# Kernel optimization log

Measured on AMD Instinct MI355X. Metric: run time of the kernel, lower is better.

The kernel has to match this reference:

```python
import jax, jax.numpy as jnp
import numpy as np

B, N, HID, EPOCH = 16, 512, 32, 201


def setup_inputs() -> dict:
    key = jax.random.key(0)
    k1, k2, k3, k4 = jax.random.split(key, 4)
    f = jax.random.normal(k1, (B, 1, N, N), dtype=jnp.float32)
    # per-sample 3x3 stencil: perturbed 5-point Laplacian, positive center for stable Jacobi
    base = jnp.array([[0., -1., 0.], [-1., 4., -1.], [0., -1., 0.]], dtype=jnp.float32)
    kernelA = base[None, None] + 0.1 * jax.random.normal(k2, (B, 1, 3, 3), dtype=jnp.float32)
    kernelA = kernelA.at[:, :, 1, 1].set(jnp.maximum(kernelA[:, :, 1, 1], 1.0))
    u = jnp.zeros((B, 1, N, N), jnp.float32)
    # stand-in DeepONet H: pointwise 2 -> HID -> 1 MLP on concat(LFA, residual)
    W1 = 0.1 * jax.random.normal(k3, (HID, 2), dtype=jnp.float32)
    b1 = jnp.zeros((HID,), jnp.float32)
    W2 = 0.1 * jax.random.normal(k4, (1, HID), dtype=jnp.float32)
    b2 = jnp.zeros((1,), jnp.float32)
    return {"f": f, "kernelA": kernelA, "u": u, "W1": W1, "b1": b1, "W2": W2, "b2": b2, "epoch": EPOCH}


def _A(x, kernel):
    # per-sample 3x3 stencil: batch dim mapped to channels, grouped conv (groups = B)
    bsz = x.shape[0]
    y = jax.lax.conv_general_dilated(
        jnp.transpose(x, (1, 0, 2, 3)), kernel, (1, 1), ((1, 1), (1, 1)),
        dimension_numbers=("NCHW", "OIHW", "NCHW"), feature_group_count=bsz)
    return jnp.transpose(y, (1, 0, 2, 3))


def _lfa(kernelA, n):
    # ComputeSmootherFactor: Jacobi symbol |prod_j (1 - tau * A_hat(theta))| on the frequency grid
    h = 1.0 / (n + 1)
    p = np.arange(-(n // 2), n // 2)
    P1, P2 = np.meshgrid(p, p)
    t1 = jnp.asarray(2j * np.pi * h * P1, jnp.complex64)
    t2 = jnp.asarray(2j * np.pi * h * P2, jnp.complex64)
    E = jnp.stack([
        jnp.exp(-t1 - t2), jnp.exp(-t2), jnp.exp(t1 - t2),
        jnp.exp(-t1), jnp.ones_like(t1), jnp.exp(t1),
        jnp.exp(-t1 + t2), jnp.exp(t2), jnp.exp(t1 + t2)])  # [9,N,N]
    bsz = kernelA.shape[0]
    S = jnp.einsum("bk,kxy->bxy", kernelA.reshape(bsz, 9).astype(jnp.complex64), E)
    tau = (0.5 / kernelA[:, 0, 1, 1]).astype(jnp.complex64)[:, None, None]
    y = (1.0 - tau * S) ** 5  # 5 identical Jacobi factors
    return jnp.abs(y)[:, None].astype(jnp.float32)  # [B,1,N,N]


def _H(lfa, r, W1, b1, W2, b2):
    # pointwise MLP correction operator (stand-in for DeepONet)
    z = jnp.concatenate([lfa, r], axis=1)  # [B,2,N,N]
    hdn = jax.nn.gelu(jnp.einsum("bcxy,oc->boxy", z, W1) + b1[None, :, None, None])
    return jnp.einsum("bcxy,oc->boxy", hdn, W2) + b2[None, :, None, None]


def reference(f, kernelA, u, W1, b1, W2, b2, epoch):
    K = (epoch - 1) // 100 + 1
    n = f.shape[-1]
    lfa = _lfa(kernelA, n)
    taus = 0.5 / kernelA[:, :, 1:2, 1:2]  # [B,1,1,1], w=0.5
    x = jnp.zeros_like(f)
    for _ in range(K):
        for _ in range(10):  # jacobi, M=10
            x = x + taus * (f - _A(x, kernelA))
        r = f - _A(x, kernelA)
        x = x + _H(lfa, r, W1, b1, W2, b2)
    r = f - _A(x, kernelA)
    return jnp.linalg.norm(r) / jnp.linalg.norm(f)
```

## Files before the change

kernel.cpp:

```cpp
#include <hip/hip_runtime.h>
#include <math.h>

#define BB 16
#define NN 512
#define HID 32

#define HALO 16
#define TW 96
#define TWP 97
#define OT 64

#define GELU_K1 (-2.302208201f)
#define GELU_K2 (-0.102944244f)

#define TPH 0.012247925f
#define CDR 0.99992499f
#define SDR 0.012247618f

__global__ __launch_bounds__(256) void lfa_kernel(const float* __restrict__ kernelA,
                                                  float* __restrict__ lfa) {
    const int t = threadIdx.x;
    const int strip = t & 127;
    const int i = blockIdx.y * 2 + (t >> 7);
    const int b = blockIdx.z;
    const int j0 = strip * 4;
    const float* a = kernelA + b * 9;
    float a0 = a[0], a1 = a[1], a2 = a[2], a3 = a[3], a4 = a[4];
    float a5 = a[5], a6 = a[6], a7 = a[7], a8 = a[8];
    const float A35 = a3 + a5, A17 = a1 + a7, A08 = a0 + a8, A26 = a2 + a6;
    const float B53 = a5 - a3, B71 = a7 - a1, B80 = a8 - a0, B26 = a2 - a6;
    const float tau = 0.5f / a4;

    float th2 = TPH * (float)(i - NN / 2);
    float th1 = TPH * (float)(j0 - NN / 2);
    float s1, c1, s2, c2;
    sincosf(th1, &s1, &c1);
    sincosf(th2, &s2, &c2);

    float out[4];
#pragma unroll
    for (int k = 0; k < 4; ++k) {
        float cc = c1 * c2, ss = s1 * s2, sc = s1 * c2, cs = c1 * s2;
        float cpp = cc - ss, cpm = cc + ss, spp = sc + cs, spm = sc - cs;
        float re = fmaf(A35, c1, a4); re = fmaf(A17, c2, re);
        re = fmaf(A08, cpp, re);      re = fmaf(A26, cpm, re);
        float im = B53 * s1;          im = fmaf(B71, s2, im);
        im = fmaf(B80, spp, im);      im = fmaf(B26, spm, im);
        float zre = fmaf(-tau, re, 1.0f);
        float zim = tau * im;
        float m2 = fmaf(zre, zre, zim * zim);
        out[k] = m2 * m2 * sqrtf(m2);
        float tt = s1 * SDR;
        float ns = fmaf(s1, CDR, c1 * SDR);
        c1 = fmaf(c1, CDR, -tt);
        s1 = ns;
    }
    float4 ov = {out[0], out[1], out[2], out[3]};
    *(float4*)(lfa + (size_t)b * NN * NN + (size_t)i * NN + j0) = ov;
}

template <bool FIRST>
__global__ __launch_bounds__(256) void fused_cycle(
        const float* __restrict__ xin, float* __restrict__ xout,
        const float* __restrict__ f, const float* __restrict__ kernelA,
        const float* __restrict__ lfa,
        const float* __restrict__ W1, const float* __restrict__ b1,
        const float* __restrict__ W2, const float* __restrict__ b2) {
    __shared__ float sxraw[98 * TWP + 2];
    float* sx = sxraw + TWP + 1;
    const int tx = threadIdx.x;
    const int ty = threadIdx.y;
    const int t  = ty * 32 + tx;
    const int b  = blockIdx.z;
    const int gy0 = blockIdx.y * OT;
    const int gx0 = blockIdx.x * OT;
    const int goi = gy0 - HALO;
    const int goj = gx0 - HALO;
    const float* fg = f + (size_t)b * NN * NN;
    const float* ag = kernelA + b * 9;
    const float ar0 = ag[0], ar1 = ag[1], ar2 = ag[2], ar3 = ag[3], ar4 = ag[4];
    const float ar5 = ag[5], ar6 = ag[6], ar7 = ag[7], ar8 = ag[8];
    const float tau = 0.5f / ar4;
    const float s0 = tau * ar0, q1 = tau * ar1, q2 = tau * ar2, q3 = tau * ar3;
    const float q4 = tau * ar4, q5 = tau * ar5, q6 = tau * ar6, q7 = tau * ar7;
    const float q8 = tau * ar8;

    if (t < 98) sxraw[t] = 0.f;
    if (t < 96) sxraw[97 + 97 * t] = 0.f;
    if (t < 98) sxraw[9409 + t] = 0.f;

    if (!FIRST) {
        const float* xg = xin + (size_t)b * NN * NN;
#pragma unroll
        for (int k = 0; k < (TW * TW) / 256; ++k) {
            int idx = t + k * 256;
            int row = idx / TW, col = idx - row * TW;
            int gi = goi + row, gj = goj + col;
            float v = 0.f;
            if (gi >= 0 && gi < NN && gj >= 0 && gj < NN) v = xg[gi * NN + gj];
            sx[row * TWP + col] = v;
        }
    }

    const int R0 = ty * 12, C0 = tx * 3;

    const float* pb  = sx + (R0 - 1) * TWP + (C0 - 1);
    float*       pwv = sx + R0 * TWP + C0;

    float vR[12], vC[3];
#pragma unroll
    for (int r = 0; r < 12; ++r) {
        int R = R0 + r, gi = goi + R;
        vR[r] = (R >= 1 && R < TW - 1 && gi >= 0 && gi < NN) ? 1.f : 0.f;
    }
#pragma unroll
    for (int c = 0; c < 3; ++c) {
        int C = C0 + c, gj = goj + C;
        vC[c] = (C >= 1 && C < TW - 1 && gj >= 0 && gj < NN) ? 1.f : 0.f;
    }

    float frt[12][3];
#pragma unroll
    for (int r = 0; r < 12; ++r) {
        int gi = goi + R0 + r;
#pragma unroll
        for (int c = 0; c < 3; ++c) {
            int gj = goj + C0 + c;
            frt[r][c] = (gi >= 0 && gi < NN && gj >= 0 && gj < NN)
                            ? tau * fg[gi * NN + gj] : 0.f;
        }
    }

    __syncthreads();

    float cur[12][3];
    if (FIRST) {
#pragma unroll
        for (int r = 0; r < 12; ++r) {
#pragma unroll
            for (int c = 0; c < 3; ++c)
                cur[r][c] = (vR[r] * vC[c]) * frt[r][c];
        }
        pwv[0] = cur[0][0]; pwv[1] = cur[0][1]; pwv[2] = cur[0][2];
        pwv[11 * TWP] = cur[11][0]; pwv[11 * TWP + 1] = cur[11][1];
        pwv[11 * TWP + 2] = cur[11][2];
#pragma unroll
        for (int r = 1; r < 11; ++r) {
            pwv[r * TWP] = cur[r][0];
            pwv[r * TWP + 2] = cur[r][2];
        }
        __syncthreads();
    } else {
#pragma unroll
        for (int r = 0; r < 12; ++r) {
            cur[r][0] = pwv[r * TWP];
            cur[r][1] = pwv[r * TWP + 1];
            cur[r][2] = pwv[r * TWP + 2];
        }
    }

    for (int s = FIRST ? 1 : 0; s < 10; ++s) {
        float top0 = pb[0], top1 = pb[1], top2 = pb[2], top3 = pb[3], top4 = pb[4];
        float bot0 = pb[13 * TWP],     bot1 = pb[13 * TWP + 1],
              bot2 = pb[13 * TWP + 2], bot3 = pb[13 * TWP + 3],
              bot4 = pb[13 * TWP + 4];
        float pm0 = top1, pm1v = top2, pm2 = top3;
        float Lm1 = top0, Rm1 = top4;
        float Lc = pb[TWP], Rc = pb[TWP + 4];
#pragma unroll
        for (int r = 0; r < 12; ++r) {
            float n0, n1, n2, Lp, Rp;
            if (r < 11) {
                n0 = cur[r + 1][0]; n1 = cur[r + 1][1]; n2 = cur[r + 1][2];
                Lp = pb[(r + 2) * TWP];
                Rp = pb[(r + 2) * TWP + 4];
            } else {
                n0 = bot1; n1 = bot2; n2 = bot3; Lp = bot0; Rp = bot4;
            }
            float o0 = cur[r][0], o1 = cur[r][1], o2 = cur[r][2];
            {
                float ax = s0 * Lm1;
                ax = fmaf(q1, pm0, ax); ax = fmaf(q2, pm1v, ax);
                ax = fmaf(q3, Lc, ax);  ax = fmaf(q4, o0, ax);
                ax = fmaf(q5, o1, ax);  ax = fmaf(q6, Lp, ax);
                ax = fmaf(q7, n0, ax);  ax = fmaf(q8, n1, ax);
                cur[r][0] = fmaf(vR[r] * vC[0], frt[r][0] - ax, o0);
            }
            {
                float ax = s0 * pm0;
                ax = fmaf(q1, pm1v, ax); ax = fmaf(q2, pm2, ax);
                ax = fmaf(q3, o0, ax);   ax = fmaf(q4, o1, ax);
                ax = fmaf(q5, o2, ax);   ax = fmaf(q6, n0, ax);
                ax = fmaf(q7, n1, ax);   ax = fmaf(q8, n2, ax);
                cur[r][1] = fmaf(vR[r] * vC[1], frt[r][1] - ax, o1);
            }
            {
                float ax = s0 * pm1v;
                ax = fmaf(q1, pm2, ax); ax = fmaf(q2, Rm1, ax);
                ax = fmaf(q3, o1, ax);  ax = fmaf(q4, o2, ax);
                ax = fmaf(q5, Rc, ax);  ax = fmaf(q6, n1, ax);
                ax = fmaf(q7, n2, ax);  ax = fmaf(q8, Rp, ax);
                cur[r][2] = fmaf(vR[r] * vC[2], frt[r][2] - ax, o2);
            }
            pm0 = o0; pm1v = o1; pm2 = o2;
            Lm1 = Lc; Rm1 = Rc; Lc = Lp; Rc = Rp;
        }
        __syncthreads();
        if (s < 9) {
            pwv[0] = cur[0][0]; pwv[1] = cur[0][1]; pwv[2] = cur[0][2];
            pwv[11 * TWP] = cur[11][0]; pwv[11 * TWP + 1] = cur[11][1];
            pwv[11 * TWP + 2] = cur[11][2];
#pragma unroll
            for (int r = 1; r < 11; ++r) {
                pwv[r * TWP] = cur[r][0];
                pwv[r * TWP + 2] = cur[r][2];
            }
        } else {
#pragma unroll
            for (int r = 0; r < 12; ++r) {
                pwv[r * TWP] = cur[r][0];
                pwv[r * TWP + 1] = cur[r][1];
                pwv[r * TWP + 2] = cur[r][2];
            }
        }
        __syncthreads();
    }

    const int orow = t >> 2;
    const int oseg = t & 3;
    const int Rl = HALO + orow;
    const int Cl0 = HALO + oseg * 16;
    const float* pw = sx + (Rl - 1) * TWP + (Cl0 - 1);
    float w0[18], w1[18], w2[18];
#pragma unroll
    for (int k = 0; k < 18; ++k) {
        w0[k] = pw[k];
        w1[k] = pw[TWP + k];
        w2[k] = pw[2 * TWP + k];
    }
    const int gi = gy0 + orow;
    const int gjb = gx0 + oseg * 16;
    const float4* f4 = (const float4*)(fg + (size_t)gi * NN + gjb);
    const float4* l4 = (const float4*)(lfa + (size_t)b * NN * NN + (size_t)gi * NN + gjb);
    float fv[16], lv[16];
#pragma unroll
    for (int q = 0; q < 4; ++q) {
        float4 fq = f4[q], lq = l4[q];
        fv[q * 4] = fq.x; fv[q * 4 + 1] = fq.y; fv[q * 4 + 2] = fq.z; fv[q * 4 + 3] = fq.w;
        lv[q * 4] = lq.x; lv[q * 4 + 1] = lq.y; lv[q * 4 + 2] = lq.z; lv[q * 4 + 3] = lq.w;
    }
    float rv[16];
#pragma unroll
    for (int k = 0; k < 16; ++k) {
        float ax = ar0 * w0[k];
        ax = fmaf(ar1, w0[k + 1], ax); ax = fmaf(ar2, w0[k + 2], ax);
        ax = fmaf(ar3, w1[k], ax);     ax = fmaf(ar4, w1[k + 1], ax);
        ax = fmaf(ar5, w1[k + 2], ax); ax = fmaf(ar6, w2[k], ax);
        ax = fmaf(ar7, w2[k + 1], ax); ax = fmaf(ar8, w2[k + 2], ax);
        rv[k] = fv[k] - ax;
    }
    float acc[16];
#pragma unroll
    for (int k = 0; k < 16; ++k) acc[k] = 0.f;
    for (int hh = 0; hh < HID; ++hh) {
        float w1a = W1[2 * hh], w1b = W1[2 * hh + 1], bb = b1[hh], wo = W2[hh];
#pragma unroll
        for (int k = 0; k < 16; ++k) {
            float v = fmaf(w1a, lv[k], fmaf(w1b, rv[k], bb));
            float m = v * fmaf(GELU_K2, v * v, GELU_K1);
            float e = __builtin_amdgcn_exp2f(m);
            float g = v * __builtin_amdgcn_rcpf(1.0f + e);
            acc[k] = fmaf(wo, g, acc[k]);
        }
    }
    const float b2v = b2[0];
    float4* xo4 = (float4*)(xout + (size_t)b * NN * NN + (size_t)gi * NN + gjb);
#pragma unroll
    for (int q = 0; q < 4; ++q) {
        float4 ov;
        ov.x = w1[q * 4 + 1] + acc[q * 4] + b2v;
        ov.y = w1[q * 4 + 2] + acc[q * 4 + 1] + b2v;
        ov.z = w1[q * 4 + 3] + acc[q * 4 + 2] + b2v;
        ov.w = w1[q * 4 + 4] + acc[q * 4 + 3] + b2v;
        xo4[q] = ov;
    }
}

__global__ __launch_bounds__(256) void resnorm_kernel(const float* __restrict__ xin,
                                                      const float* __restrict__ f,
                                                      const float* __restrict__ kernelA,
                                                      float* __restrict__ acc) {
    const int total_strips = BB * NN * (NN / 4);
    float rr = 0.f, f2 = 0.f;
    for (int p = blockIdx.x * 256 + threadIdx.x; p < total_strips;
         p += gridDim.x * 256) {
        int b = p >> 16;
        int rem = p & 65535;
        int i = rem >> 7;
        int js = (rem & 127) << 2;
        const float* a = kernelA + b * 9;
        const float* x = xin + (size_t)b * NN * NN;

        float4 up = {0,0,0,0}, mid, dn = {0,0,0,0};
        float upl = 0.f, upr = 0.f, midl = 0.f, midr = 0.f, dnl = 0.f, dnr = 0.f;
        const float* rowm = x + (size_t)i * NN + js;
        mid = *(const float4*)rowm;
        if (js > 0)       midl = rowm[-1];
        if (js + 4 < NN)  midr = rowm[4];
        if (i > 0) {
            const float* rowu = rowm - NN;
            up = *(const float4*)rowu;
            if (js > 0)      upl = rowu[-1];
            if (js + 4 < NN) upr = rowu[4];
        }
        if (i + 1 < NN) {
            const float* rowd = rowm + NN;
            dn = *(const float4*)rowd;
            if (js > 0)      dnl = rowd[-1];
            if (js + 4 < NN) dnr = rowd[4];
        }
        float u[6] = {upl, up.x, up.y, up.z, up.w, upr};
        float m[6] = {midl, mid.x, mid.y, mid.z, mid.w, midr};
        float d[6] = {dnl, dn.x, dn.y, dn.z, dn.w, dnr};
        float4 fq = *(const float4*)(f + (size_t)b * NN * NN + (size_t)i * NN + js);
        float fvv[4] = {fq.x, fq.y, fq.z, fq.w};
#pragma unroll
        for (int c = 0; c < 4; ++c) {
            float ax = a[0] * u[c];
            ax = fmaf(a[1], u[c + 1], ax); ax = fmaf(a[2], u[c + 2], ax);
            ax = fmaf(a[3], m[c], ax);     ax = fmaf(a[4], m[c + 1], ax);
            ax = fmaf(a[5], m[c + 2], ax); ax = fmaf(a[6], d[c], ax);
            ax = fmaf(a[7], d[c + 1], ax); ax = fmaf(a[8], d[c + 2], ax);
            float r = fvv[c] - ax;
            rr = fmaf(r, r, rr);
            f2 = fmaf(fvv[c], fvv[c], f2);
        }
    }
#pragma unroll
    for (int off = 32; off > 0; off >>= 1) {
        rr += __shfl_down(rr, off, 64);
        f2 += __shfl_down(f2, off, 64);
    }
    __shared__ float sr[4], sf[4];
    int wave = threadIdx.x >> 6;
    if ((threadIdx.x & 63) == 0) { sr[wave] = rr; sf[wave] = f2; }
    __syncthreads();
    if (threadIdx.x == 0) {
        atomicAdd(&acc[0], sr[0] + sr[1] + sr[2] + sr[3]);
        atomicAdd(&acc[1], sf[0] + sf[1] + sf[2] + sf[3]);
    }
}

__global__ void finalize_kernel(const float* __restrict__ acc, float* __restrict__ out) {
    out[0] = sqrtf(acc[0] / acc[1]);
}

extern "C" void kernel_launch(void* const* d_in, const int* in_sizes, int n_in,
                              void* d_out, int out_size, void* d_ws, size_t ws_size,
                              hipStream_t stream) {
    const float* f  = (const float*)d_in[0];
    const float* kA = (const float*)d_in[1];
    float*       u  = (float*)d_in[2];
    const float* W1 = (const float*)d_in[3];
    const float* b1 = (const float*)d_in[4];
    const float* W2 = (const float*)d_in[5];
    const float* b2 = (const float*)d_in[6];
    float* out = (float*)d_out;

    char* ws = (char*)d_ws;
    float* acc = (float*)ws;
    float* xB  = (float*)(ws + 256);
    float* lfa = (float*)(ws + 256 + (size_t)BB * NN * NN * 4);

    hipMemsetAsync(acc, 0, 2 * sizeof(float), stream);

    lfa_kernel<<<dim3(1, NN / 2, BB), 256, 0, stream>>>(kA, lfa);

    dim3 jblk(32, 8);
    dim3 jgrd(NN / OT, NN / OT, BB);

    fused_cycle<true><<<jgrd, jblk, 0, stream>>>(u, xB, f, kA, lfa, W1, b1, W2, b2);
    fused_cycle<false><<<jgrd, jblk, 0, stream>>>(xB, u, f, kA, lfa, W1, b1, W2, b2);
    fused_cycle<false><<<jgrd, jblk, 0, stream>>>(u, xB, f, kA, lfa, W1, b1, W2, b2);

    resnorm_kernel<<<2048, 256, 0, stream>>>(xB, f, kA, acc);
    finalize_kernel<<<1, 1, 0, stream>>>(acc, out);
}
```

Measured before the change: 431.2 us.

## Exchange Jacobi column halos by wave shuffles and double-buffer row halos

Left and right neighbour values in the register-tiled Jacobi sweep now come from lane shuffles instead of shared memory, so each sweep stores only the top and bottom boundary rows. Those boundary rows alternate between the main tile and a second shared-memory region, which lets each sweep drop to one barrier instead of two. This cuts LDS traffic and barrier stalls per sweep. In exchange it adds shuffle instructions and edge masking, and relies on the 32-wide thread row mapping neatly onto halves of a 64-lane wave.

```diff
diff --git a/kernel.cpp b/kernel.cpp
--- a/kernel.cpp
+++ b/kernel.cpp
@@ -86,7 +86,6 @@
     const float q8 = tau * ar8;
 
     if (t < 98) sxraw[t] = 0.f;
-    if (t < 96) sxraw[97 + 97 * t] = 0.f;
     if (t < 98) sxraw[9409 + t] = 0.f;
 
     if (!FIRST) {
@@ -106,6 +105,9 @@
 
     const float* pb  = sx + (R0 - 1) * TWP + (C0 - 1);
     float*       pwv = sx + R0 * TWP + C0;
+    float*       pwB = sx + (R0 + 1) * TWP + (C0 + 1);
+    const float* pbB  = sx + ((ty == 0) ? 1 : (R0 - 11)) * TWP + (C0 + 1);
+    const float* pbBb = sx + ((ty == 7) ? 1 : (R0 + 20)) * TWP + (C0 + 1);
 
     float vR[12], vC[3];
 #pragma unroll
@@ -141,14 +143,8 @@
             for (int c = 0; c < 3; ++c)
                 cur[r][c] = (vR[r] * vC[c]) * frt[r][c];
         }
-        pwv[0] = cur[0][0]; pwv[1] = cur[0][1]; pwv[2] = cur[0][2];
-        pwv[11 * TWP] = cur[11][0]; pwv[11 * TWP + 1] = cur[11][1];
-        pwv[11 * TWP + 2] = cur[11][2];
-#pragma unroll
-        for (int r = 1; r < 11; ++r) {
-            pwv[r * TWP] = cur[r][0];
-            pwv[r * TWP + 2] = cur[r][2];
-        }
+        pwB[7 * TWP] = cur[0][0]; pwB[8 * TWP] = cur[0][1]; pwB[9 * TWP] = cur[0][2];
+        pwB[0] = cur[11][0]; pwB[TWP] = cur[11][1]; pwB[2 * TWP] = cur[11][2];
         __syncthreads();
     } else {
 #pragma unroll
@@ -159,72 +155,103 @@
         }
     }
 
-    for (int s = FIRST ? 1 : 0; s < 10; ++s) {
-        float top0 = pb[0], top1 = pb[1], top2 = pb[2], top3 = pb[3], top4 = pb[4];
-        float bot0 = pb[13 * TWP],     bot1 = pb[13 * TWP + 1],
-              bot2 = pb[13 * TWP + 2], bot3 = pb[13 * TWP + 3],
-              bot4 = pb[13 * TWP + 4];
-        float pm0 = top1, pm1v = top2, pm2 = top3;
-        float Lm1 = top0, Rm1 = top4;
-        float Lc = pb[TWP], Rc = pb[TWP + 4];
-#pragma unroll
-        for (int r = 0; r < 12; ++r) {
-            float n0, n1, n2, Lp, Rp;
-            if (r < 11) {
-                n0 = cur[r + 1][0]; n1 = cur[r + 1][1]; n2 = cur[r + 1][2];
-                Lp = pb[(r + 2) * TWP];
-                Rp = pb[(r + 2) * TWP + 4];
-            } else {
-                n0 = bot1; n1 = bot2; n2 = bot3; Lp = bot0; Rp = bot4;
-            }
-            float o0 = cur[r][0], o1 = cur[r][1], o2 = cur[r][2];
-            {
-                float ax = s0 * Lm1;
-                ax = fmaf(q1, pm0, ax); ax = fmaf(q2, pm1v, ax);
-                ax = fmaf(q3, Lc, ax);  ax = fmaf(q4, o0, ax);
-                ax = fmaf(q5, o1, ax);  ax = fmaf(q6, Lp, ax);
-                ax = fmaf(q7, n0, ax);  ax = fmaf(q8, n1, ax);
-                cur[r][0] = fmaf(vR[r] * vC[0], frt[r][0] - ax, o0);
-            }
-            {
-                float ax = s0 * pm0;
-                ax = fmaf(q1, pm1v, ax); ax = fmaf(q2, pm2, ax);
-                ax = fmaf(q3, o0, ax);   ax = fmaf(q4, o1, ax);
-                ax = fmaf(q5, o2, ax);   ax = fmaf(q6, n0, ax);
-                ax = fmaf(q7, n1, ax);   ax = fmaf(q8, n2, ax);
-                cur[r][1] = fmaf(vR[r] * vC[1], frt[r][1] - ax, o1);
-            }
-            {
-                float ax = s0 * pm1v;
-                ax = fmaf(q1, pm2, ax); ax = fmaf(q2, Rm1, ax);
-                ax = fmaf(q3, o1, ax);  ax = fmaf(q4, o2, ax);
-                ax = fmaf(q5, Rc, ax);  ax = fmaf(q6, n1, ax);
-                ax = fmaf(q7, n2, ax);  ax = fmaf(q8, Rp, ax);
-                cur[r][2] = fmaf(vR[r] * vC[2], frt[r][2] - ax, o2);
-            }
-            pm0 = o0; pm1v = o1; pm2 = o2;
-            Lm1 = Lc; Rm1 = Rc; Lc = Lp; Rc = Rp;
-        }
-        __syncthreads();
-        if (s < 9) {
-            pwv[0] = cur[0][0]; pwv[1] = cur[0][1]; pwv[2] = cur[0][2];
-            pwv[11 * TWP] = cur[11][0]; pwv[11 * TWP + 1] = cur[11][1];
-            pwv[11 * TWP + 2] = cur[11][2];
-#pragma unroll
-            for (int r = 1; r < 11; ++r) {
-                pwv[r * TWP] = cur[r][0];
-                pwv[r * TWP + 2] = cur[r][2];
-            }
-        } else {
-#pragma unroll
-            for (int r = 0; r < 12; ++r) {
-                pwv[r * TWP] = cur[r][0];
-                pwv[r * TWP + 1] = cur[r][1];
-                pwv[r * TWP + 2] = cur[r][2];
-            }
-        }
-        __syncthreads();
-    }
+#define SWEEP(READB, FINAL_)                                                 \
+    {                                                                        \
+        float top0, top1, top2, top3, top4, bot0, bot1, bot2, bot3, bot4;    \
+        if (READB) {                                                         \
+            top0 = pbB[2 * TWP - 3]; top1 = pbB[0]; top2 = pbB[TWP];         \
+            top3 = pbB[2 * TWP];     top4 = pbB[3];                          \
+            bot0 = pbBb[2 * TWP - 3]; bot1 = pbBb[0]; bot2 = pbBb[TWP];      \
+            bot3 = pbBb[2 * TWP];     bot4 = pbBb[3];                        \
+            if (ty == 0) { top0 = 0.f; top1 = 0.f; top2 = 0.f;               \
+                           top3 = 0.f; top4 = 0.f; }                         \
+            if (ty == 7) { bot0 = 0.f; bot1 = 0.f; bot2 = 0.f;               \
+                           bot3 = 0.f; bot4 = 0.f; }                         \
+        } else {                                                             \
+            top0 = pb[0]; top1 = pb[1]; top2 = pb[2]; top3 = pb[3];          \
+            top4 = pb[4];                                                    \
+            bot0 = pb[13 * TWP];     bot1 = pb[13 * TWP + 1];                \
+            bot2 = pb[13 * TWP + 2]; bot3 = pb[13 * TWP + 3];                \
+            bot4 = pb[13 * TWP + 4];                                         \
+        }                                                                    \
+        float pm0 = top1, pm1v = top2, pm2 = top3;                           \
+        float Lm1 = top0, Rm1 = top4;                                        \
+        float Lct = __shfl_up(cur[0][2], 1, 64);                             \
+        float Rct = __shfl_down(cur[0][0], 1, 64);                           \
+        float Lc = tx ? Lct : 0.f;                                           \
+        float Rc = (tx == 31) ? 0.f : Rct;                                   \
+        _Pragma("unroll")                                                    \
+        for (int r = 0; r < 12; ++r) {                                       \
+            float n0, n1, n2, Lp, Rp;                                        \
+            if (r < 11) {                                                    \
+                n0 = cur[r + 1][0]; n1 = cur[r + 1][1]; n2 = cur[r + 1][2];  \
+                float Lpt = __shfl_up(n2, 1, 64);                            \
+                float Rpt = __shfl_down(n0, 1, 64);                          \
+                Lp = tx ? Lpt : 0.f;                                         \
+                Rp = (tx == 31) ? 0.f : Rpt;                                 \
+            } else {                                                         \
+                n0 = bot1; n1 = bot2; n2 = bot3; Lp = bot0; Rp = bot4;       \
+            }                                                                \
+            float o0 = cur[r][0], o1 = cur[r][1], o2 = cur[r][2];            \
+            {                                                                \
+                float ax = s0 * Lm1;                                         \
+                ax = fmaf(q1, pm0, ax); ax = fmaf(q2, pm1v, ax);             \
+                ax = fmaf(q3, Lc, ax);  ax = fmaf(q4, o0, ax);               \
+                ax = fmaf(q5, o1, ax);  ax = fmaf(q6, Lp, ax);               \
+                ax = fmaf(q7, n0, ax);  ax = fmaf(q8, n1, ax);               \
+                cur[r][0] = fmaf(vR[r] * vC[0], frt[r][0] - ax, o0);         \
+            }                                                                \
+            {                                                                \
+                float ax = s0 * pm0;                                         \
+                ax = fmaf(q1, pm1v, ax); ax = fmaf(q2, pm2, ax);             \
+                ax = fmaf(q3, o0, ax);   ax = fmaf(q4, o1, ax);              \
+                ax = fmaf(q5, o2, ax);   ax = fmaf(q6, n0, ax);              \
+                ax = fmaf(q7, n1, ax);   ax = fmaf(q8, n2, ax);              \
+                cur[r][1] = fmaf(vR[r] * vC[1], frt[r][1] - ax, o1);         \
+            }                                                                \
+            {                                                                \
+                float ax = s0 * pm1v;                                        \
+                ax = fmaf(q1, pm2, ax); ax = fmaf(q2, Rm1, ax);              \
+                ax = fmaf(q3, o1, ax);  ax = fmaf(q4, o2, ax);               \
+                ax = fmaf(q5, Rc, ax);  ax = fmaf(q6, n1, ax);               \
+                ax = fmaf(q7, n2, ax);  ax = fmaf(q8, Rp, ax);               \
+                cur[r][2] = fmaf(vR[r] * vC[2], frt[r][2] - ax, o2);         \
+            }                                                                \
+            pm0 = o0; pm1v = o1; pm2 = o2;                                   \
+            Lm1 = Lc; Rm1 = Rc; Lc = Lp; Rc = Rp;                            \
+        }                                                                    \
+        if (!(FINAL_)) {                                                     \
+            if (READB) {          \
+                pwv[0] = cur[0][0]; pwv[1] = cur[0][1]; pwv[2] = cur[0][2];  \
+                pwv[11 * TWP] = cur[11][0];                                  \
+                pwv[11 * TWP + 1] = cur[11][1];                              \
+                pwv[11 * TWP + 2] = cur[11][2];                              \
+            } else {                     \
+                pwB[7 * TWP] = cur[0][0]; pwB[8 * TWP] = cur[0][1];          \
+                pwB[9 * TWP] = cur[0][2];                                    \
+                pwB[0] = cur[11][0]; pwB[TWP] = cur[11][1];                  \
+                pwB[2 * TWP] = cur[11][2];                                   \
+            }                                                                \
+            __syncthreads();                                                 \
+        } else {                                                             \
+            __syncthreads();         \
+            _Pragma("unroll")                                                \
+            for (int r = 0; r < 12; ++r) {                                   \
+                pwv[r * TWP] = cur[r][0];                                    \
+                pwv[r * TWP + 1] = cur[r][1];                                \
+                pwv[r * TWP + 2] = cur[r][2];                                \
+            }                                                                \
+            __syncthreads();         \
+        }                                                                    \
+    }
+
+    if (!FIRST) SWEEP(0, 0)
+    for (int p = 0; p < 4; ++p) {
+        SWEEP(1, 0)
+        SWEEP(0, 0)
+    }
+    SWEEP(1, 1)
+#undef SWEEP
 
     const int orow = t >> 2;
     const int oseg = t & 3;
```

Result: slower. 579.6 us (+34.4%).
